# Kernel optimization log

Measured on AMD Instinct MI355X. Metric: run time of the kernel, lower is better.

## Reference

```python
import jax, jax.numpy as jnp
import numpy as np

N, E, G, D, L, EA = 100000, 1600000, 128, 128, 3, 7
BN_EPS = 1e-5


def _bn(x, g, b, m, v):
    # eval-mode BatchNorm1d with running stats
    return (x - m) * (g / jnp.sqrt(v + BN_EPS)) + b


def setup_inputs() -> dict:
    key = jax.random.key(0)
    ks = iter(jax.random.split(key, 64))
    nrm = lambda shape, s: jax.random.normal(next(ks), shape, jnp.float32) * s
    unif = lambda shape: jax.random.uniform(next(ks), shape, jnp.float32) * 0.5 + 0.5
    inp = {
        # forward tensor args
        'x': jnp.zeros((N,), jnp.int32),  # indices into Embedding(1, D) -> all zero
        'edge_index': jax.random.randint(next(ks), (2, E), 0, N, jnp.int32),
        'edge_attr': nrm((E, EA), 1.0),
        'batch': jnp.sort(jax.random.randint(next(ks), (N,), 0, G, jnp.int32)),
        # embeddings
        'node_emb': nrm((1, D), 1.0),
        'vn_emb': nrm((1, D), 0.1),
        # per-layer GINConv params (stacked on leading layer dim)
        'edge_W': nrm((L, EA, D), EA ** -0.5), 'edge_b': jnp.zeros((L, D), jnp.float32),
        'eps': jnp.zeros((L,), jnp.float32),
        'mlp_W1': nrm((L, D, 2 * D), D ** -0.5), 'mlp_b1': jnp.zeros((L, 2 * D), jnp.float32),
        'mbn_g': jnp.ones((L, 2 * D), jnp.float32), 'mbn_b': jnp.zeros((L, 2 * D), jnp.float32),
        'mbn_m': nrm((L, 2 * D), 0.1), 'mbn_v': unif((L, 2 * D)),
        'mlp_W2': nrm((L, 2 * D, D), (2 * D) ** -0.5), 'mlp_b2': jnp.zeros((L, D), jnp.float32),
        # outer per-layer BatchNorm
        'bn_g': jnp.ones((L, D), jnp.float32), 'bn_b': jnp.zeros((L, D), jnp.float32),
        'bn_m': nrm((L, D), 0.1), 'bn_v': unif((L, D)),
        # virtual-node MLPs (L-1 of them)
        'vn_W1': nrm((L - 1, D, 2 * D), D ** -0.5), 'vn_b1': jnp.zeros((L - 1, 2 * D), jnp.float32),
        'vbn1_g': jnp.ones((L - 1, 2 * D), jnp.float32), 'vbn1_b': jnp.zeros((L - 1, 2 * D), jnp.float32),
        'vbn1_m': nrm((L - 1, 2 * D), 0.1), 'vbn1_v': unif((L - 1, 2 * D)),
        'vn_W2': nrm((L - 1, 2 * D, D), (2 * D) ** -0.5), 'vn_b2': jnp.zeros((L - 1, D), jnp.float32),
        'vbn2_g': jnp.ones((L - 1, D), jnp.float32), 'vbn2_b': jnp.zeros((L - 1, D), jnp.float32),
        'vbn2_m': nrm((L - 1, D), 0.1), 'vbn2_v': unif((L - 1, D)),
    }
    return inp


def reference(x, edge_index, edge_attr, batch, node_emb, vn_emb,
              edge_W, edge_b, eps, mlp_W1, mlp_b1, mbn_g, mbn_b, mbn_m, mbn_v,
              mlp_W2, mlp_b2, bn_g, bn_b, bn_m, bn_v,
              vn_W1, vn_b1, vbn1_g, vbn1_b, vbn1_m, vbn1_v,
              vn_W2, vn_b2, vbn2_g, vbn2_b, vbn2_m, vbn2_v):
    src, dst = edge_index[0], edge_index[1]
    h = node_emb[x]                                # [N, D] node encoder gather
    vn = jnp.broadcast_to(vn_emb[0], (G, D))       # virtual node per graph
    for l in range(L):
        h_in = h + vn[batch]                       # broadcast virtual node to nodes
        # GINConv
        e = edge_attr @ edge_W[l] + edge_b[l]      # [E, D]
        msg = jax.nn.relu(h_in[src] + e)           # gather + edge fuse
        agg = jax.ops.segment_sum(msg, dst, num_segments=N)
        z = (1.0 + eps[l]) * h_in + agg
        z = jax.nn.relu(_bn(z @ mlp_W1[l] + mlp_b1[l], mbn_g[l], mbn_b[l], mbn_m[l], mbn_v[l]))
        h2 = z @ mlp_W2[l] + mlp_b2[l]
        # outer BatchNorm (+ relu except last layer; dropout is identity in eval)
        h2 = _bn(h2, bn_g[l], bn_b[l], bn_m[l], bn_v[l])
        h = h2 if l == L - 1 else jax.nn.relu(h2)
        if l < L - 1:
            vt = jax.ops.segment_sum(h_in, batch, num_segments=G) + vn  # global_add_pool
            t = jax.nn.relu(_bn(vt @ vn_W1[l] + vn_b1[l], vbn1_g[l], vbn1_b[l], vbn1_m[l], vbn1_v[l]))
            vn = jax.nn.relu(_bn(t @ vn_W2[l] + vn_b2[l], vbn2_g[l], vbn2_b[l], vbn2_m[l], vbn2_v[l]))
    return h  # JK == 'last'
```

## Files before the change

kernel.cpp:

```cpp
#include <hip/hip_runtime.h>
#include <hip/hip_bf16.h>

#define NN 100000
#define NP 100032
#define EE 1600000
#define GG 128
#define DD 128
#define LL 3
#define EAA 7
#define BN_EPS 1e-5f

typedef __attribute__((ext_vector_type(8))) short bf16x8;
typedef __attribute__((ext_vector_type(4))) float f32x4;
typedef __attribute__((ext_vector_type(4))) unsigned short u16x4;
typedef _Float16 f16x2 __attribute__((ext_vector_type(2)));

__device__ __forceinline__ unsigned short f2bf(float x) {
    unsigned int u = __float_as_uint(x);
    u = (u + 0x7FFF + ((u >> 16) & 1)) >> 16;
    return (unsigned short)u;
}
__device__ __forceinline__ float bf2f(unsigned short h) {
    return __uint_as_float(((unsigned int)h) << 16);
}
__device__ __forceinline__ float bflo(unsigned int u) {
    return __uint_as_float(u << 16);
}
__device__ __forceinline__ float bfhi(unsigned int u) {
    return __uint_as_float(u & 0xFFFF0000u);
}
__device__ __forceinline__ unsigned int pkf16(float a, float b) {
    f16x2 v = {(_Float16)a, (_Float16)b};
    return __builtin_bit_cast(unsigned int, v);
}
__device__ __forceinline__ unsigned short f16bits(float a) {
    _Float16 h = (_Float16)a;
    return __builtin_bit_cast(unsigned short, h);
}

#if __has_builtin(__builtin_amdgcn_fdot2)
#define DOT2(q, w, c) __builtin_amdgcn_fdot2((q), (w), (c), false)
#else
__device__ __forceinline__ float dot2_sw(f16x2 a, f16x2 b, float c) {
    return fmaf((float)a.x, (float)b.x, fmaf((float)a.y, (float)b.y, c));
}
#define DOT2(q, w, c) dot2_sw((q), (w), (c))
#endif

__global__ __launch_bounds__(256) void init_kernel(
    const int* __restrict__ x, const float* __restrict__ node_emb,
    const float* __restrict__ vn_emb, float* __restrict__ h,
    float* __restrict__ vn)
{
    long i = (long)blockIdx.x * 256 + threadIdx.x;
    if (i < (long)NN * DD) {
        int node = (int)(i >> 7), d = (int)(i & 127);
        h[i] = node_emb[(long)x[node] * DD + d];
    }
    if (i < GG * DD) vn[i] = vn_emb[i & 127];
}

#define R1 8
__global__ __launch_bounds__(256) void hin_kernel(
    float* __restrict__ hbuf,
    unsigned short* __restrict__ h16,
    const float* __restrict__ vn,
    const int* __restrict__ batch,
    const float* __restrict__ eps,
    float* __restrict__ agg,
    float* __restrict__ vt,
    int layer, int accum_vt, int write_agg)
{
    const int d  = threadIdx.x & 127;
    const int rg = threadIdx.x >> 7;
    const float epl = 1.0f + eps[layer];
    const long row0 = (long)blockIdx.x * (R1 * 2);

    float vacc = 0.0f;
    int   vb   = -1;
    #pragma unroll
    for (int r = 0; r < R1; ++r) {
        long row = row0 + rg + 2 * r;
        if (row >= NN) break;
        int b = batch[row];
        long idx = row * DD + d;
        float hv = hbuf[idx] + vn[(long)b * DD + d];
        hbuf[idx] = hv;
        h16[idx]  = f2bf(hv);
        if (write_agg) agg[idx] = epl * hv;
        if (accum_vt) {
            if (b != vb) {
                if (vb >= 0) atomicAdd(&vt[(long)vb * DD + d], vacc);
                vb = b; vacc = 0.0f;
            }
            vacc += hv;
        }
    }
    if (accum_vt && vb >= 0) atomicAdd(&vt[(long)vb * DD + d], vacc);
}

__global__ __launch_bounds__(256) void vt_kernel(
    const float* __restrict__ hbuf, const int* __restrict__ batch,
    float* __restrict__ vt)
{
    const int d  = threadIdx.x & 127;
    const int rg = threadIdx.x >> 7;
    const long row0 = (long)blockIdx.x * 16;
    float vacc = 0.0f;
    int   vb   = -1;
    #pragma unroll
    for (int r = 0; r < 8; ++r) {
        long row = row0 + rg + 2 * r;
        if (row >= NN) break;
        int b = batch[row];
        float hv = hbuf[row * DD + d];
        if (b != vb) {
            if (vb >= 0) atomicAdd(&vt[(long)vb * DD + d], vacc);
            vb = b; vacc = 0.0f;
        }
        vacc += hv;
    }
    if (vb >= 0) atomicAdd(&vt[(long)vb * DD + d], vacc);
}

__global__ __launch_bounds__(256) void cnt_kernel(
    const int* __restrict__ batch, int* __restrict__ cnt)
{
    const int tid = blockIdx.x * 256 + threadIdx.x;
    const int CH  = (NN + 16383) / 16384;
    long s = (long)tid * CH;
    long e = s + CH; if (e > NN) e = NN;
    int vb = -1, c = 0;
    for (long i = s; i < e; ++i) {
        int b = batch[i];
        if (b != vb) { if (vb >= 0) atomicAdd(&cnt[vb], c); vb = b; c = 0; }
        ++c;
    }
    if (vb >= 0) atomicAdd(&cnt[vb], c);
}

__global__ __launch_bounds__(256) void count_kernel(
    const int* __restrict__ ei, int* __restrict__ deg)
{
    long e = (long)blockIdx.x * 256 + threadIdx.x;
    if (e < EE) atomicAdd(&deg[ei[EE + e]], 1);
}

__global__ __launch_bounds__(1024) void scan_a(
    const int* __restrict__ deg, int* __restrict__ rp, int* __restrict__ partials)
{
    __shared__ int s[1024];
    int t = threadIdx.x;
    long i = (long)blockIdx.x * 1024 + t;
    int v = (i < NN) ? deg[i] : 0;
    s[t] = v;
    __syncthreads();
    for (int off = 1; off < 1024; off <<= 1) {
        int u = (t >= off) ? s[t - off] : 0;
        __syncthreads();
        s[t] += u;
        __syncthreads();
    }
    if (i < NN) rp[i] = s[t] - v;
    if (t == 1023) partials[blockIdx.x] = s[1023];
}

__global__ void scan_b(int* __restrict__ partials, int nb)
{
    if (threadIdx.x == 0) {
        int run = 0;
        for (int i = 0; i < nb; ++i) { int v = partials[i]; partials[i] = run; run += v; }
    }
}

__global__ __launch_bounds__(1024) void scan_c(
    int* __restrict__ rp, int* __restrict__ fill, const int* __restrict__ partials)
{
    long i = (long)blockIdx.x * 1024 + threadIdx.x;
    if (i < NN) {
        int v = rp[i] + partials[blockIdx.x];
        rp[i] = v;
        fill[i] = v;
    }
    if (i == 0) rp[NN] = EE;
}

__global__ __launch_bounds__(256) void scatter_kernel(
    const int* __restrict__ ei, const float* __restrict__ eattr,
    int* __restrict__ fill, unsigned int* __restrict__ attr16,
    int* __restrict__ eid_perm)
{
    long e = (long)blockIdx.x * 256 + threadIdx.x;
    if (e >= EE) return;
    int dst = ei[EE + e];
    int pos = atomicAdd(&fill[dst], 1);
    if (attr16) {
        unsigned int src = (unsigned int)ei[e];
        uint4 w;
        w.x = pkf16(eattr[e * EAA + 0], eattr[e * EAA + 1]);
        w.y = pkf16(eattr[e * EAA + 2], eattr[e * EAA + 3]);
        w.z = pkf16(eattr[e * EAA + 4], eattr[e * EAA + 5]);
        unsigned int a6 = (unsigned int)f16bits(eattr[e * EAA + 6]) & 0xFFFEu;
        w.w = a6 | ((src >> 16) & 1u) | (src << 16);
        *(uint4*)(attr16 + (long)pos * 4) = w;
    } else {
        eid_perm[pos] = (int)e;
    }
}

#define WPAIR_PREAMBLE(eWl)                                                   \
    f16x2 wx[4], wy[4];                                                       \
    {                                                                         \
        _Pragma("unroll")                                                     \
        for (int j = 0; j < 3; ++j) {                                         \
            float2 p0 = *(const float2*)&(eWl)[(2 * j) * DD + d0];            \
            float2 p1 = *(const float2*)&(eWl)[(2 * j + 1) * DD + d0];        \
            wx[j] = (f16x2){(_Float16)p0.x, (_Float16)p1.x};                  \
            wy[j] = (f16x2){(_Float16)p0.y, (_Float16)p1.y};                  \
        }                                                                     \
        float2 p6 = *(const float2*)&(eWl)[6 * DD + d0];                      \
        wx[3] = (f16x2){(_Float16)p6.x, (_Float16)0.0f};                      \
        wy[3] = (f16x2){(_Float16)p6.y, (_Float16)0.0f};                      \
    }

#define EDOT(AU, EX, EY)                                                      \
    float EX = bias.x, EY = bias.y;                                           \
    {                                                                         \
        f16x2 q0 = __builtin_bit_cast(f16x2, AU.x);                           \
        f16x2 q1 = __builtin_bit_cast(f16x2, AU.y);                           \
        f16x2 q2 = __builtin_bit_cast(f16x2, AU.z);                           \
        f16x2 q3 = __builtin_bit_cast(f16x2, AU.w & 0x0000FFFEu);             \
        EX = DOT2(q0, wx[0], EX); EY = DOT2(q0, wy[0], EY);                   \
        EX = DOT2(q1, wx[1], EX); EY = DOT2(q1, wy[1], EY);                   \
        EX = DOT2(q2, wx[2], EX); EY = DOT2(q2, wy[2], EY);                   \
        EX = DOT2(q3, wx[3], EX); EY = DOT2(q3, wy[3], EY);                   \
    }

#define UNPACK_SRC(AW) (int)(((AW) >> 16) | (((AW) & 1u) << 16))

__global__ __launch_bounds__(256) void gin0_kernel(
    const float* __restrict__ node_emb,
    const float* __restrict__ vn_emb,
    const int* __restrict__ rp,
    const unsigned int* __restrict__ attr16,
    const float* __restrict__ eW, const float* __restrict__ eb,
    const float* __restrict__ eps,
    unsigned short* __restrict__ aggh, unsigned short* __restrict__ aggl)
{
    const int lane = threadIdx.x & 63;
    const int wid  = __builtin_amdgcn_readfirstlane(threadIdx.x >> 6);
    const int n    = blockIdx.x * 4 + wid;
    const int d0   = lane * 2;

    WPAIR_PREAMBLE(eW)
    const float2 bias = *(const float2*)&eb[d0];
    const float  epl  = 1.0f + eps[0];

    const float cx = node_emb[d0]     + vn_emb[d0];
    const float cy = node_emb[d0 + 1] + vn_emb[d0 + 1];
    float accx = epl * cx, accy = epl * cy;

    int p        = __builtin_amdgcn_readfirstlane(rp[n]);
    const int p1 = __builtin_amdgcn_readfirstlane(rp[n + 1]);

    #define EDGE0(AU)                                                         \
    {                                                                         \
        EDOT(AU, ex, ey)                                                      \
        float mx = cx + ex, my = cy + ey;                                     \
        accx += fmaxf(mx, 0.0f); accy += fmaxf(my, 0.0f);                     \
    }

    for (; p + 4 <= p1; p += 4) {
        const uint4* a4p = (const uint4*)(attr16 + (long)p * 4);
        uint4 A0 = a4p[0];
        uint4 A1 = a4p[1];
        uint4 A2 = a4p[2];
        uint4 A3 = a4p[3];
        EDGE0(A0)
        EDGE0(A1)
        EDGE0(A2)
        EDGE0(A3)
    }
    for (; p < p1; ++p) {
        uint4 A = *(const uint4*)(attr16 + (long)p * 4);
        EDGE0(A)
    }
    #undef EDGE0

    unsigned short hx = f2bf(accx), hy = f2bf(accy);
    *(unsigned int*)&aggh[(long)n * DD + d0] = (unsigned int)hx | ((unsigned int)hy << 16);
    *(unsigned int*)&aggl[(long)n * DD + d0] =
        (unsigned int)f2bf(accx - bf2f(hx)) | ((unsigned int)f2bf(accy - bf2f(hy)) << 16);
}

__global__ __launch_bounds__(256) void gin_agg_kernel(
    const float* __restrict__ h_in,
    const unsigned short* __restrict__ h16,
    const int* __restrict__ rp,
    const unsigned int* __restrict__ attr16,
    const float* __restrict__ eW, const float* __restrict__ eb,
    const float* __restrict__ eps,
    unsigned short* __restrict__ aggh, unsigned short* __restrict__ aggl,
    int layer)
{
    const int lane = threadIdx.x & 63;
    const int wid  = __builtin_amdgcn_readfirstlane(threadIdx.x >> 6);
    const int n    = blockIdx.x * 4 + wid;
    const int d0   = lane * 2;

    const float* eWl = eW + (long)layer * EAA * DD;
    WPAIR_PREAMBLE(eWl)
    const float2 bias = *(const float2*)&eb[layer * DD + d0];
    const float  epl  = 1.0f + eps[layer];

    float2 hn = *(const float2*)&h_in[(long)n * DD + d0];
    float accx = epl * hn.x, accy = epl * hn.y;

    int p        = __builtin_amdgcn_readfirstlane(rp[n]);
    const int p1 = __builtin_amdgcn_readfirstlane(rp[n + 1]);

    #define EDGE(AU, GU)                                                      \
    {                                                                         \
        EDOT(AU, ex, ey)                                                      \
        float mx = bflo(GU) + ex, my = bfhi(GU) + ey;                         \
        accx += fmaxf(mx, 0.0f); accy += fmaxf(my, 0.0f);                     \
    }

    for (; p + 4 <= p1; p += 4) {
        const uint4* a4p = (const uint4*)(attr16 + (long)p * 4);
        uint4 A0 = a4p[0];
        uint4 A1 = a4p[1];
        uint4 A2 = a4p[2];
        uint4 A3 = a4p[3];
        int s0 = __builtin_amdgcn_readfirstlane(UNPACK_SRC(A0.w));
        int s1 = __builtin_amdgcn_readfirstlane(UNPACK_SRC(A1.w));
        int s2 = __builtin_amdgcn_readfirstlane(UNPACK_SRC(A2.w));
        int s3 = __builtin_amdgcn_readfirstlane(UNPACK_SRC(A3.w));
        unsigned int g0 = *(const unsigned int*)(h16 + (long)s0 * DD + d0);
        unsigned int g1 = *(const unsigned int*)(h16 + (long)s1 * DD + d0);
        unsigned int g2 = *(const unsigned int*)(h16 + (long)s2 * DD + d0);
        unsigned int g3 = *(const unsigned int*)(h16 + (long)s3 * DD + d0);
        EDGE(A0, g0)
        EDGE(A1, g1)
        EDGE(A2, g2)
        EDGE(A3, g3)
    }
    for (; p < p1; ++p) {
        uint4 A = *(const uint4*)(attr16 + (long)p * 4);
        int s = __builtin_amdgcn_readfirstlane(UNPACK_SRC(A.w));
        unsigned int g = *(const unsigned int*)(h16 + (long)s * DD + d0);
        EDGE(A, g)
    }
    #undef EDGE

    unsigned short hx = f2bf(accx), hy = f2bf(accy);
    *(unsigned int*)&aggh[(long)n * DD + d0] = (unsigned int)hx | ((unsigned int)hy << 16);
    *(unsigned int*)&aggl[(long)n * DD + d0] =
        (unsigned int)f2bf(accx - bf2f(hx)) | ((unsigned int)f2bf(accy - bf2f(hy)) << 16);
}

__global__ __launch_bounds__(256) void gin_agg_eid_kernel(
    const float* __restrict__ h_in,
    const int* __restrict__ rp,
    const int* __restrict__ eid_perm,
    const int* __restrict__ ei,
    const float* __restrict__ eattr,
    const float* __restrict__ eW, const float* __restrict__ eb,
    const float* __restrict__ eps,
    float* __restrict__ agg, int layer)
{
    const int d    = threadIdx.x & 127;
    const int half = threadIdx.x >> 7;
    const long n   = (long)blockIdx.x * 2 + half;

    float w[EAA];
    #pragma unroll
    for (int a = 0; a < EAA; ++a) w[a] = eW[layer * EAA * DD + a * DD + d];
    const float bias = eb[layer * DD + d];
    const float epl  = 1.0f + eps[layer];

    float acc = epl * h_in[n * DD + d];
    const int p0 = rp[n], p1 = rp[n + 1];
    for (int p = p0; p < p1; ++p) {
        int e = eid_perm[p];
        int src = ei[e];
        float ea = bias;
        #pragma unroll
        for (int a = 0; a < EAA; ++a)
            ea = fmaf(eattr[(long)e * EAA + a], w[a], ea);
        float m = h_in[(long)src * DD + d] + ea;
        acc += m > 0.0f ? m : 0.0f;
    }
    agg[n * DD + d] = acc;
}

__global__ __launch_bounds__(256) void wprep_kernel(
    const float* __restrict__ W1, const float* __restrict__ W2,
    unsigned short* __restrict__ w1h, unsigned short* __restrict__ w1l,
    unsigned short* __restrict__ w2h, unsigned short* __restrict__ w2l)
{
    int tid = blockIdx.x * 256 + threadIdx.x;
    if (tid >= LL * 2 * 32768) return;
    int l = tid / 65536;
    int rem = tid - l * 65536;
    int mat = rem >> 15;
    int fi = rem & 32767;
    int b = fi & 7, lane = (fi >> 3) & 63;
    int kgrp = ((lane >> 4) << 3) + b;
    if (mat == 0) {
        int mt = (fi >> 9) & 15, kk = fi >> 13;
        int m = (mt << 4) + (lane & 15);
        int k = (kk << 5) + kgrp;
        float v = W1[(long)l * DD * 2 * DD + (long)k * 2 * DD + m];
        unsigned short hi = f2bf(v);
        w1h[(long)l * 32768 + fi] = hi;
        w1l[(long)l * 32768 + fi] = f2bf(v - bf2f(hi));
    } else {
        int mt = (fi >> 9) & 7, kk = fi >> 12;
        int m = (mt << 4) + (lane & 15);
        int k = (kk << 5) + kgrp;
        float v = W2[(long)l * 2 * DD * DD + (long)k * DD + m];
        unsigned short hi = f2bf(v);
        w2h[(long)l * 32768 + fi] = hi;
        w2l[(long)l * 32768 + fi] = f2bf(v - bf2f(hi));
    }
}

__global__ __launch_bounds__(256) void bnprep_kernel(
    const float* __restrict__ b1, const float* __restrict__ g1,
    const float* __restrict__ be1, const float* __restrict__ m1,
    const float* __restrict__ v1,
    const float* __restrict__ b2, const float* __restrict__ g2,
    const float* __restrict__ be2, const float* __restrict__ m2,
    const float* __restrict__ v2,
    float* __restrict__ sc1, float* __restrict__ sh1,
    float* __restrict__ sc2, float* __restrict__ sh2)
{
    int tid = blockIdx.x * 256 + threadIdx.x;
    if (tid < LL * 2 * DD) {
        float sc = g1[tid] / sqrtf(v1[tid] + BN_EPS);
        sc1[tid] = sc;
        sh1[tid] = (b1[tid] - m1[tid]) * sc + be1[tid];
    }
    int t2 = tid - LL * 2 * DD;
    if (t2 >= 0 && t2 < LL * DD) {
        float sc = g2[t2] / sqrtf(v2[t2] + BN_EPS);
        sc2[t2] = sc;
        sh2[t2] = (b2[t2] - m2[t2]) * sc + be2[t2];
    }
}

__global__ __launch_bounds__(256, 2) void mlp_mfma_kernel(
    const float* __restrict__ z_in,
    const unsigned short* __restrict__ z16h, const unsigned short* __restrict__ z16l,
    int zfmt,
    const unsigned short* __restrict__ w1h, const unsigned short* __restrict__ w1l,
    const unsigned short* __restrict__ w2h, const unsigned short* __restrict__ w2l,
    const float* __restrict__ sc1, const float* __restrict__ sh1,
    const float* __restrict__ sc2, const float* __restrict__ sh2,
    float* __restrict__ h_out, int layer, int do_relu,
    const int* __restrict__ batch, const float* __restrict__ vnbuf,
    unsigned short* __restrict__ h16, int fuse)
{
    __shared__ char lds[65536];
    const int tid  = threadIdx.x;
    const int lane = tid & 63;
    const int wv   = tid >> 6;
    const long row0 = (long)blockIdx.x * 64;
    const int kb = (lane >> 4) << 3;

    if (zfmt) {
        const uint4* zh = (const uint4*)(z16h + row0 * DD);
        const uint4* zl = (const uint4*)(z16l + row0 * DD);
        #pragma unroll
        for (int i = 0; i < 4; ++i) {
            int idx = tid + i * 256;
            uint4 hv = zh[idx];
            uint4 lv = zl[idx];
            int r = idx >> 4;
            int c = (idx & 15) << 3;
            int off = ((r << 8) + (c << 1)) ^ ((r & 7) << 4);
            *(uint4*)(lds + off)         = hv;
            *(uint4*)(lds + 16384 + off) = lv;
        }
    } else {
        const float4* zi = (const float4*)(z_in + row0 * DD);
        #pragma unroll
        for (int i = 0; i < 8; ++i) {
            int idx = tid + i * 256;
            float4 v = zi[idx];
            int r = idx >> 5;
            int c = (idx & 31) << 2;
            u16x4 hv, lv;
            hv.x = f2bf(v.x); lv.x = f2bf(v.x - bf2f(hv.x));
            hv.y = f2bf(v.y); lv.y = f2bf(v.y - bf2f(hv.y));
            hv.z = f2bf(v.z); lv.z = f2bf(v.z - bf2f(hv.z));
            hv.w = f2bf(v.w); lv.w = f2bf(v.w - bf2f(hv.w));
            int off = ((r << 8) + (c << 1)) ^ ((r & 7) << 4);
            *(u16x4*)(lds + off)         = hv;
            *(u16x4*)(lds + 16384 + off) = lv;
        }
    }
    __syncthreads();

    bf16x8 B1h[4][4], B1l[4][4];
    #pragma unroll
    for (int nt = 0; nt < 4; ++nt) {
        int r = (nt << 4) + (lane & 15);
        #pragma unroll
        for (int kk = 0; kk < 4; ++kk) {
            int off = ((r << 8) + (((kk << 5) + kb) << 1)) ^ ((r & 7) << 4);
            B1h[nt][kk] = *(const bf16x8*)(lds + off);
            B1l[nt][kk] = *(const bf16x8*)(lds + 16384 + off);
        }
    }
    __syncthreads();

    const unsigned short* w1hl = w1h + (long)layer * 32768;
    const unsigned short* w1ll = w1l + (long)layer * 32768;
    #pragma unroll
    for (int mtl = 0; mtl < 4; ++mtl) {
        const int mt = (wv << 2) + mtl;
        bf16x8 Ah[4], Al[4];
        #pragma unroll
        for (int kk = 0; kk < 4; ++kk) {
            const long boff = ((long)((kk << 4) + mt) * 64 + lane) << 3;
            Ah[kk] = *(const bf16x8*)(w1hl + boff);
            Al[kk] = *(const bf16x8*)(w1ll + boff);
        }
        f32x4 acc[4];
        #pragma unroll
        for (int nt = 0; nt < 4; ++nt) acc[nt] = (f32x4){0.f, 0.f, 0.f, 0.f};
        #pragma unroll
        for (int kk = 0; kk < 4; ++kk) {
            #pragma unroll
            for (int nt = 0; nt < 4; ++nt) {
                acc[nt] = __builtin_amdgcn_mfma_f32_16x16x32_bf16(Ah[kk], B1h[nt][kk], acc[nt], 0, 0, 0);
                acc[nt] = __builtin_amdgcn_mfma_f32_16x16x32_bf16(Ah[kk], B1l[nt][kk], acc[nt], 0, 0, 0);
                acc[nt] = __builtin_amdgcn_mfma_f32_16x16x32_bf16(Al[kk], B1h[nt][kk], acc[nt], 0, 0, 0);
            }
        }
        const int m0 = (mt << 4) + ((lane >> 4) << 2);
        const float4 s4 = *(const float4*)&sc1[layer * 2 * DD + m0];
        const float4 t4 = *(const float4*)&sh1[layer * 2 * DD + m0];
        #pragma unroll
        for (int nt = 0; nt < 4; ++nt) {
            int row = (nt << 4) + (lane & 15);
            float u0 = fmaxf(fmaf(acc[nt][0], s4.x, t4.x), 0.0f);
            float u1 = fmaxf(fmaf(acc[nt][1], s4.y, t4.y), 0.0f);
            float u2 = fmaxf(fmaf(acc[nt][2], s4.z, t4.z), 0.0f);
            float u3 = fmaxf(fmaf(acc[nt][3], s4.w, t4.w), 0.0f);
            u16x4 hv, lv;
            hv.x = f2bf(u0); lv.x = f2bf(u0 - bf2f(hv.x));
            hv.y = f2bf(u1); lv.y = f2bf(u1 - bf2f(hv.y));
            hv.z = f2bf(u2); lv.z = f2bf(u2 - bf2f(hv.z));
            hv.w = f2bf(u3); lv.w = f2bf(u3 - bf2f(hv.w));
            int off = ((row << 9) + (m0 << 1)) ^ ((row & 7) << 4);
            *(u16x4*)(lds + off)         = hv;
            *(u16x4*)(lds + 32768 + off) = lv;
        }
    }
    __syncthreads();

    const unsigned short* w2hl = w2h + (long)layer * 32768;
    const unsigned short* w2ll = w2l + (long)layer * 32768;
    f32x4 acc2[2][4];
    #pragma unroll
    for (int mtl = 0; mtl < 2; ++mtl)
        #pragma unroll
        for (int nt = 0; nt < 4; ++nt) acc2[mtl][nt] = (f32x4){0.f, 0.f, 0.f, 0.f};

    #pragma unroll
    for (int kk = 0; kk < 8; ++kk) {
        bf16x8 Bh[4], Bl[4];
        #pragma unroll
        for (int nt = 0; nt < 4; ++nt) {
            int r = (nt << 4) + (lane & 15);
            int off = ((r << 9) + (((kk << 5) + kb) << 1)) ^ ((r & 7) << 4);
            Bh[nt] = *(const bf16x8*)(lds + off);
            Bl[nt] = *(const bf16x8*)(lds + 32768 + off);
        }
        #pragma unroll
        for (int mtl = 0; mtl < 2; ++mtl) {
            const int mt = (wv << 1) + mtl;
            const long boff = ((long)((kk << 3) + mt) * 64 + lane) << 3;
            bf16x8 Ah = *(const bf16x8*)(w2hl + boff);
            bf16x8 Al = *(const bf16x8*)(w2ll + boff);
            #pragma unroll
            for (int nt = 0; nt < 4; ++nt) {
                acc2[mtl][nt] = __builtin_amdgcn_mfma_f32_16x16x32_bf16(Ah, Bh[nt], acc2[mtl][nt], 0, 0, 0);
                acc2[mtl][nt] = __builtin_amdgcn_mfma_f32_16x16x32_bf16(Ah, Bl[nt], acc2[mtl][nt], 0, 0, 0);
                acc2[mtl][nt] = __builtin_amdgcn_mfma_f32_16x16x32_bf16(Al, Bh[nt], acc2[mtl][nt], 0, 0, 0);
            }
        }
    }
    #pragma unroll
    for (int mtl = 0; mtl < 2; ++mtl) {
        const int m0 = ((((wv << 1) + mtl)) << 4) + ((lane >> 4) << 2);
        const float4 s4 = *(const float4*)&sc2[layer * DD + m0];
        const float4 t4 = *(const float4*)&sh2[layer * DD + m0];
        #pragma unroll
        for (int nt = 0; nt < 4; ++nt) {
            long row = row0 + (nt << 4) + (lane & 15);
            if (row < NN) {
                float o0 = fmaf(acc2[mtl][nt][0], s4.x, t4.x);
                float o1 = fmaf(acc2[mtl][nt][1], s4.y, t4.y);
                float o2 = fmaf(acc2[mtl][nt][2], s4.z, t4.z);
                float o3 = fmaf(acc2[mtl][nt][3], s4.w, t4.w);
                if (do_relu) {
                    o0 = fmaxf(o0, 0.0f); o1 = fmaxf(o1, 0.0f);
                    o2 = fmaxf(o2, 0.0f); o3 = fmaxf(o3, 0.0f);
                }
                if (fuse) {
                    int b = batch[row];
                    float4 vnv = *(const float4*)&vnbuf[(long)b * DD + m0];
                    o0 += vnv.x; o1 += vnv.y; o2 += vnv.z; o3 += vnv.w;
                    u16x4 hv;
                    hv.x = f2bf(o0); hv.y = f2bf(o1);
                    hv.z = f2bf(o2); hv.w = f2bf(o3);
                    *(u16x4*)&h16[row * DD + m0] = hv;
                }
                *(float4*)&h_out[row * DD + m0] = make_float4(o0, o1, o2, o3);
            }
        }
    }
}

__global__ __launch_bounds__(256) void vn_kernel(
    const float* __restrict__ vt, float* __restrict__ vn,
    const float* __restrict__ W1, const float* __restrict__ b1,
    const float* __restrict__ g1, const float* __restrict__ be1,
    const float* __restrict__ m1, const float* __restrict__ v1,
    const float* __restrict__ W2, const float* __restrict__ b2,
    const float* __restrict__ g2, const float* __restrict__ be2,
    const float* __restrict__ m2, const float* __restrict__ v2,
    int layer)
{
    __shared__ float row[DD];
    __shared__ float u[2 * DD];
    const int g = blockIdx.x;
    const int t = threadIdx.x;

    if (t < DD) row[t] = vt[(long)g * DD + t] + vn[(long)g * DD + t];
    __syncthreads();

    {
        const float* W = W1 + (long)layer * DD * 2 * DD;
        float acc = 0.0f;
        for (int k = 0; k < DD; ++k) acc = fmaf(row[k], W[k * 2 * DD + t], acc);
        const long o = (long)layer * 2 * DD + t;
        float sc = g1[o] / sqrtf(v1[o] + BN_EPS);
        float sh = be1[o] - m1[o] * sc;
        float val = (acc + b1[o]) * sc + sh;
        u[t] = val > 0.0f ? val : 0.0f;
    }
    __syncthreads();

    if (t < DD) {
        const float* W = W2 + (long)layer * 2 * DD * DD;
        float acc = 0.0f;
        for (int k = 0; k < 2 * DD; ++k) acc = fmaf(u[k], W[k * DD + t], acc);
        const long o = (long)layer * DD + t;
        float sc = g2[o] / sqrtf(v2[o] + BN_EPS);
        float sh = be2[o] - m2[o] * sc;
        float val = (acc + b2[o]) * sc + sh;
        vn[(long)g * DD + t] = val > 0.0f ? val : 0.0f;
    }
}

__global__ __launch_bounds__(256) void vn0_kernel(
    const int* __restrict__ cnt,
    const float* __restrict__ node_emb, const float* __restrict__ vn_emb,
    float* __restrict__ vn,
    const float* __restrict__ W1, const float* __restrict__ b1,
    const float* __restrict__ g1, const float* __restrict__ be1,
    const float* __restrict__ m1, const float* __restrict__ v1,
    const float* __restrict__ W2, const float* __restrict__ b2,
    const float* __restrict__ g2, const float* __restrict__ be2,
    const float* __restrict__ m2, const float* __restrict__ v2)
{
    __shared__ float row[DD];
    __shared__ float u[2 * DD];
    const int g = blockIdx.x;
    const int t = threadIdx.x;

    if (t < DD) {
        float c = node_emb[t] + vn_emb[t];
        row[t] = (float)cnt[g] * c + vn_emb[t];
    }
    __syncthreads();

    {
        float acc = 0.0f;
        for (int k = 0; k < DD; ++k) acc = fmaf(row[k], W1[k * 2 * DD + t], acc);
        float sc = g1[t] / sqrtf(v1[t] + BN_EPS);
        float sh = be1[t] - m1[t] * sc;
        float val = (acc + b1[t]) * sc + sh;
        u[t] = val > 0.0f ? val : 0.0f;
    }
    __syncthreads();

    if (t < DD) {
        float acc = 0.0f;
        for (int k = 0; k < 2 * DD; ++k) acc = fmaf(u[k], W2[k * DD + t], acc);
        float sc = g2[t] / sqrtf(v2[t] + BN_EPS);
        float sh = be2[t] - m2[t] * sc;
        float val = (acc + b2[t]) * sc + sh;
        vn[(long)g * DD + t] = val > 0.0f ? val : 0.0f;
    }
}

extern "C" void kernel_launch(void* const* d_in, const int* in_sizes, int n_in,
                              void* d_out, int out_size, void* d_ws, size_t ws_size,
                              hipStream_t stream)
{
    const int*   x       = (const int*)  d_in[0];
    const int*   ei      = (const int*)  d_in[1];
    const float* eattr   = (const float*)d_in[2];
    const int*   batch   = (const int*)  d_in[3];
    const float* node_emb= (const float*)d_in[4];
    const float* vn_emb  = (const float*)d_in[5];
    const float* edge_W  = (const float*)d_in[6];
    const float* edge_b  = (const float*)d_in[7];
    const float* eps     = (const float*)d_in[8];
    const float* mlp_W1  = (const float*)d_in[9];
    const float* mlp_b1  = (const float*)d_in[10];
    const float* mbn_g   = (const float*)d_in[11];
    const float* mbn_b   = (const float*)d_in[12];
    const float* mbn_m   = (const float*)d_in[13];
    const float* mbn_v   = (const float*)d_in[14];
    const float* mlp_W2  = (const float*)d_in[15];
    const float* mlp_b2  = (const float*)d_in[16];
    const float* bn_g    = (const float*)d_in[17];
    const float* bn_b    = (const float*)d_in[18];
    const float* bn_m    = (const float*)d_in[19];
    const float* bn_v    = (const float*)d_in[20];
    const float* vn_W1   = (const float*)d_in[21];
    const float* vn_b1   = (const float*)d_in[22];
    const float* vbn1_g  = (const float*)d_in[23];
    const float* vbn1_b  = (const float*)d_in[24];
    const float* vbn1_m  = (const float*)d_in[25];
    const float* vbn1_v  = (const float*)d_in[26];
    const float* vn_W2   = (const float*)d_in[27];
    const float* vn_b2   = (const float*)d_in[28];
    const float* vbn2_g  = (const float*)d_in[29];
    const float* vbn2_b  = (const float*)d_in[30];
    const float* vbn2_m  = (const float*)d_in[31];
    const float* vbn2_v  = (const float*)d_in[32];

    float* h = (float*)d_out;
    char*  ws = (char*)d_ws;

    size_t off = 0;
    auto alloc = [&](size_t bytes) -> void* {
        void* p = ws + off;
        off += (bytes + 255) & ~(size_t)255;
        return p;
    };
    const size_t GDB = (size_t)GG * DD * sizeof(float);

    float* agg      = (float*)alloc((size_t)NP * DD * sizeof(float));
    unsigned short* aggh = (unsigned short*)agg;
    unsigned short* aggl = aggh + (size_t)NP * DD;
    unsigned short* h16 = (unsigned short*)alloc((size_t)NN * DD * sizeof(unsigned short));
    float* vn       = (float*)alloc(GDB);
    float* vt       = (float*)alloc(GDB);
    int*   rp       = (int*)  alloc((NN + 1) * sizeof(int));
    int*   fill     = (int*)  alloc(NN * sizeof(int));
    int*   partials = (int*)  alloc(128 * sizeof(int));
    int*   cnt      = (int*)  alloc(GG * sizeof(int));
    unsigned short* w1h = (unsigned short*)alloc(LL * 32768 * sizeof(unsigned short));
    unsigned short* w1l = (unsigned short*)alloc(LL * 32768 * sizeof(unsigned short));
    unsigned short* w2h = (unsigned short*)alloc(LL * 32768 * sizeof(unsigned short));
    unsigned short* w2l = (unsigned short*)alloc(LL * 32768 * sizeof(unsigned short));
    float* bn1sc = (float*)alloc(LL * 2 * DD * sizeof(float));
    float* bn1sh = (float*)alloc(LL * 2 * DD * sizeof(float));
    float* bn2sc = (float*)alloc(LL * DD * sizeof(float));
    float* bn2sh = (float*)alloc(LL * DD * sizeof(float));
    const size_t base_end = off;

    unsigned int* attr16 = nullptr;
    int* eid_perm = nullptr;
    if (ws_size >= base_end + (size_t)EE * 4 * sizeof(unsigned int))
        attr16 = (unsigned int*)alloc((size_t)EE * 4 * sizeof(unsigned int));
    else if (ws_size >= base_end + (size_t)EE * sizeof(int))
        eid_perm = (int*)alloc((size_t)EE * sizeof(int));
    const bool csr = (attr16 != nullptr) || (eid_perm != nullptr);

    wprep_kernel<<<(LL * 2 * 32768 + 255) / 256, 256, 0, stream>>>(
        mlp_W1, mlp_W2, w1h, w1l, w2h, w2l);
    bnprep_kernel<<<(LL * 2 * DD + LL * DD + 255) / 256, 256, 0, stream>>>(
        mlp_b1, mbn_g, mbn_b, mbn_m, mbn_v,
        mlp_b2, bn_g, bn_b, bn_m, bn_v,
        bn1sc, bn1sh, bn2sc, bn2sh);

    if (csr) {
        const int egrid = (EE + 255) / 256;
        const int ngrid = (NN + 1023) / 1024;
        hipMemsetAsync(fill, 0, NN * sizeof(int), stream);
        count_kernel<<<egrid, 256, 0, stream>>>(ei, fill);
        scan_a<<<ngrid, 1024, 0, stream>>>(fill, rp, partials);
        scan_b<<<1, 64, 0, stream>>>(partials, ngrid);
        scan_c<<<ngrid, 1024, 0, stream>>>(rp, fill, partials);
        scatter_kernel<<<egrid, 256, 0, stream>>>(ei, eattr, fill, attr16, eid_perm);
    }

    if (attr16) {
        hipMemsetAsync(cnt, 0, GG * sizeof(int), stream);
        cnt_kernel<<<64, 256, 0, stream>>>(batch, cnt);

        vn0_kernel<<<GG, 256, 0, stream>>>(
            cnt, node_emb, vn_emb, vn,
            vn_W1, vn_b1, vbn1_g, vbn1_b, vbn1_m, vbn1_v,
            vn_W2, vn_b2, vbn2_g, vbn2_b, vbn2_m, vbn2_v);
        gin0_kernel<<<NN / 4, 256, 0, stream>>>(
            node_emb, vn_emb, rp, attr16, edge_W, edge_b, eps, aggh, aggl);
        mlp_mfma_kernel<<<NP / 64, 256, 0, stream>>>(
            agg, aggh, aggl, 1, w1h, w1l, w2h, w2l, bn1sc, bn1sh, bn2sc, bn2sh,
            h, 0, 1, batch, vn, h16, 1);

        hipMemsetAsync(vt, 0, GDB, stream);
        vt_kernel<<<NN / 16, 256, 0, stream>>>(h, batch, vt);
        vn_kernel<<<GG, 256, 0, stream>>>(
            vt, vn, vn_W1, vn_b1, vbn1_g, vbn1_b, vbn1_m, vbn1_v,
            vn_W2, vn_b2, vbn2_g, vbn2_b, vbn2_m, vbn2_v, 1);
        gin_agg_kernel<<<NN / 4, 256, 0, stream>>>(
            h, h16, rp, attr16, edge_W, edge_b, eps, aggh, aggl, 1);
        mlp_mfma_kernel<<<NP / 64, 256, 0, stream>>>(
            agg, aggh, aggl, 1, w1h, w1l, w2h, w2l, bn1sc, bn1sh, bn2sc, bn2sh,
            h, 1, 1, batch, vn, h16, 1);

        gin_agg_kernel<<<NN / 4, 256, 0, stream>>>(
            h, h16, rp, attr16, edge_W, edge_b, eps, aggh, aggl, 2);
        mlp_mfma_kernel<<<NP / 64, 256, 0, stream>>>(
            agg, aggh, aggl, 1, w1h, w1l, w2h, w2l, bn1sc, bn1sh, bn2sc, bn2sh,
            h, 2, 0, batch, vn, h16, 0);
    } else {
        {
            long total = (long)NN * DD;
            init_kernel<<<(int)((total + 255) / 256), 256, 0, stream>>>(
                x, node_emb, vn_emb, h, vn);
        }
        for (int l = 0; l < LL; ++l) {
            int accum = (l < LL - 1) ? 1 : 0;
            if (accum)
                hipMemsetAsync(vt, 0, GDB, stream);

            hin_kernel<<<NN / (R1 * 2), 256, 0, stream>>>(
                h, h16, vn, batch, eps, agg, vt, l, accum, 1);

            if (eid_perm) {
                gin_agg_eid_kernel<<<NN / 2, 256, 0, stream>>>(
                    h, rp, eid_perm, ei, eattr, edge_W, edge_b, eps, agg, l);
            }

            mlp_mfma_kernel<<<NP / 64, 256, 0, stream>>>(
                agg, nullptr, nullptr, 0, w1h, w1l, w2h, w2l,
                bn1sc, bn1sh, bn2sc, bn2sh,
                h, l, accum, batch, vn, h16, 0);

            if (accum)
                vn_kernel<<<GG, 256, 0, stream>>>(
                    vt, vn, vn_W1, vn_b1, vbn1_g, vbn1_b, vbn1_m, vbn1_v,
                    vn_W2, vn_b2, vbn2_g, vbn2_b, vbn2_m, vbn2_v, l);
        }
    }
}
```

Before: 662.1 us.

## Bin CSR edge scatter by destination range and store source ids separately

Replaces the single-pass edge scatter with a binned scatter. Each block walks one chunk of edges and only handles edges whose destination falls in one of 8 node ranges, so the atomics and scattered writes for a block stay within a small region of memory that is more likely to stay in cache. Source indices now go to their own int array instead of being bit-packed into the edge-attribute word, and the aggregation kernel reads them with a vector load. In exchange, the destination array is read eight times, and each aggregation layer does an extra index load per edge.

Measured after the change: 657.0 us. No clear change (-0.8%).

```diff
diff --git a/kernel.cpp b/kernel.cpp
--- a/kernel.cpp
+++ b/kernel.cpp
@@ -9,6 +9,8 @@
 #define LL 3
 #define EAA 7
 #define BN_EPS 1e-5f
+#define NBIN 8
+#define BINW 12500
 
 typedef __attribute__((ext_vector_type(8))) short bf16x8;
 typedef __attribute__((ext_vector_type(4))) float f32x4;
@@ -32,10 +34,6 @@
 __device__ __forceinline__ unsigned int pkf16(float a, float b) {
     f16x2 v = {(_Float16)a, (_Float16)b};
     return __builtin_bit_cast(unsigned int, v);
-}
-__device__ __forceinline__ unsigned short f16bits(float a) {
-    _Float16 h = (_Float16)a;
-    return __builtin_bit_cast(unsigned short, h);
 }
 
 #if __has_builtin(__builtin_amdgcn_fdot2)
@@ -185,27 +183,40 @@
     if (i == 0) rp[NN] = EE;
 }
 
-__global__ __launch_bounds__(256) void scatter_kernel(
+#define P2C 8192
+__global__ __launch_bounds__(256) void binscat_kernel(
     const int* __restrict__ ei, const float* __restrict__ eattr,
-    int* __restrict__ fill, unsigned int* __restrict__ attr16,
+    int* __restrict__ fill,
+    unsigned int* __restrict__ attr16, int* __restrict__ src_arr)
+{
+    const int b  = blockIdx.x & 7;
+    const long e0 = (long)(blockIdx.x >> 3) * P2C;
+    const int lo = b * BINW, hi = lo + BINW;
+    long e1 = e0 + P2C; if (e1 > EE) e1 = EE;
+    for (long e = e0 + threadIdx.x; e < e1; e += 256) {
+        int dst = ei[EE + e];
+        if (dst >= lo && dst < hi) {
+            int q = atomicAdd(&fill[dst], 1);
+            uint4 w;
+            w.x = pkf16(eattr[e * EAA + 0], eattr[e * EAA + 1]);
+            w.y = pkf16(eattr[e * EAA + 2], eattr[e * EAA + 3]);
+            w.z = pkf16(eattr[e * EAA + 4], eattr[e * EAA + 5]);
+            w.w = pkf16(eattr[e * EAA + 6], 0.0f);
+            *(uint4*)(attr16 + (long)q * 4) = w;
+            src_arr[q] = ei[e];
+        }
+    }
+}
+
+__global__ __launch_bounds__(256) void scatter_eid_kernel(
+    const int* __restrict__ ei, int* __restrict__ fill,
     int* __restrict__ eid_perm)
 {
     long e = (long)blockIdx.x * 256 + threadIdx.x;
     if (e >= EE) return;
     int dst = ei[EE + e];
     int pos = atomicAdd(&fill[dst], 1);
-    if (attr16) {
-        unsigned int src = (unsigned int)ei[e];
-        uint4 w;
-        w.x = pkf16(eattr[e * EAA + 0], eattr[e * EAA + 1]);
-        w.y = pkf16(eattr[e * EAA + 2], eattr[e * EAA + 3]);
-        w.z = pkf16(eattr[e * EAA + 4], eattr[e * EAA + 5]);
-        unsigned int a6 = (unsigned int)f16bits(eattr[e * EAA + 6]) & 0xFFFEu;
-        w.w = a6 | ((src >> 16) & 1u) | (src << 16);
-        *(uint4*)(attr16 + (long)pos * 4) = w;
-    } else {
-        eid_perm[pos] = (int)e;
-    }
+    eid_perm[pos] = (int)e;
 }
 
 #define WPAIR_PREAMBLE(eWl)                                                   \
@@ -229,14 +240,12 @@
         f16x2 q0 = __builtin_bit_cast(f16x2, AU.x);                           \
         f16x2 q1 = __builtin_bit_cast(f16x2, AU.y);                           \
         f16x2 q2 = __builtin_bit_cast(f16x2, AU.z);                           \
-        f16x2 q3 = __builtin_bit_cast(f16x2, AU.w & 0x0000FFFEu);             \
+        f16x2 q3 = __builtin_bit_cast(f16x2, AU.w);                           \
         EX = DOT2(q0, wx[0], EX); EY = DOT2(q0, wy[0], EY);                   \
         EX = DOT2(q1, wx[1], EX); EY = DOT2(q1, wy[1], EY);                   \
         EX = DOT2(q2, wx[2], EX); EY = DOT2(q2, wy[2], EY);                   \
         EX = DOT2(q3, wx[3], EX); EY = DOT2(q3, wy[3], EY);                   \
     }
-
-#define UNPACK_SRC(AW) (int)(((AW) >> 16) | (((AW) & 1u) << 16))
 
 __global__ __launch_bounds__(256) void gin0_kernel(
     const float* __restrict__ node_emb,
@@ -298,6 +307,7 @@
     const unsigned short* __restrict__ h16,
     const int* __restrict__ rp,
     const unsigned int* __restrict__ attr16,
+    const int* __restrict__ src_arr,
     const float* __restrict__ eW, const float* __restrict__ eb,
     const float* __restrict__ eps,
     unsigned short* __restrict__ aggh, unsigned short* __restrict__ aggl,
@@ -327,15 +337,16 @@
     }
 
     for (; p + 4 <= p1; p += 4) {
+        int4 sv = *(const int4*)(src_arr + p);
+        int s0 = __builtin_amdgcn_readfirstlane(sv.x);
+        int s1 = __builtin_amdgcn_readfirstlane(sv.y);
+        int s2 = __builtin_amdgcn_readfirstlane(sv.z);
+        int s3 = __builtin_amdgcn_readfirstlane(sv.w);
         const uint4* a4p = (const uint4*)(attr16 + (long)p * 4);
         uint4 A0 = a4p[0];
         uint4 A1 = a4p[1];
         uint4 A2 = a4p[2];
         uint4 A3 = a4p[3];
-        int s0 = __builtin_amdgcn_readfirstlane(UNPACK_SRC(A0.w));
-        int s1 = __builtin_amdgcn_readfirstlane(UNPACK_SRC(A1.w));
-        int s2 = __builtin_amdgcn_readfirstlane(UNPACK_SRC(A2.w));
-        int s3 = __builtin_amdgcn_readfirstlane(UNPACK_SRC(A3.w));
         unsigned int g0 = *(const unsigned int*)(h16 + (long)s0 * DD + d0);
         unsigned int g1 = *(const unsigned int*)(h16 + (long)s1 * DD + d0);
         unsigned int g2 = *(const unsigned int*)(h16 + (long)s2 * DD + d0);
@@ -346,8 +357,8 @@
         EDGE(A3, g3)
     }
     for (; p < p1; ++p) {
+        int s = __builtin_amdgcn_readfirstlane(src_arr[p]);
         uint4 A = *(const uint4*)(attr16 + (long)p * 4);
-        int s = __builtin_amdgcn_readfirstlane(UNPACK_SRC(A.w));
         unsigned int g = *(const unsigned int*)(h16 + (long)s * DD + d0);
         EDGE(A, g)
     }
@@ -769,6 +780,7 @@
     int*   fill     = (int*)  alloc(NN * sizeof(int));
     int*   partials = (int*)  alloc(128 * sizeof(int));
     int*   cnt      = (int*)  alloc(GG * sizeof(int));
+    int*   src_arr  = (int*)  alloc((size_t)EE * sizeof(int));
     unsigned short* w1h = (unsigned short*)alloc(LL * 32768 * sizeof(unsigned short));
     unsigned short* w1l = (unsigned short*)alloc(LL * 32768 * sizeof(unsigned short));
     unsigned short* w2h = (unsigned short*)alloc(LL * 32768 * sizeof(unsigned short));
@@ -780,12 +792,9 @@
     const size_t base_end = off;
 
     unsigned int* attr16 = nullptr;
-    int* eid_perm = nullptr;
     if (ws_size >= base_end + (size_t)EE * 4 * sizeof(unsigned int))
         attr16 = (unsigned int*)alloc((size_t)EE * 4 * sizeof(unsigned int));
-    else if (ws_size >= base_end + (size_t)EE * sizeof(int))
-        eid_perm = (int*)alloc((size_t)EE * sizeof(int));
-    const bool csr = (attr16 != nullptr) || (eid_perm != nullptr);
+    int* eid_perm = src_arr;
 
     wprep_kernel<<<(LL * 2 * 32768 + 255) / 256, 256, 0, stream>>>(
         mlp_W1, mlp_W2, w1h, w1l, w2h, w2l);
@@ -794,7 +803,7 @@
         mlp_b2, bn_g, bn_b, bn_m, bn_v,
         bn1sc, bn1sh, bn2sc, bn2sh);
 
-    if (csr) {
+    {
         const int egrid = (EE + 255) / 256;
         const int ngrid = (NN + 1023) / 1024;
         hipMemsetAsync(fill, 0, NN * sizeof(int), stream);
@@ -802,7 +811,13 @@
         scan_a<<<ngrid, 1024, 0, stream>>>(fill, rp, partials);
         scan_b<<<1, 64, 0, stream>>>(partials, ngrid);
         scan_c<<<ngrid, 1024, 0, stream>>>(rp, fill, partials);
-        scatter_kernel<<<egrid, 256, 0, stream>>>(ei, eattr, fill, attr16, eid_perm);
+        if (attr16) {
+            const int chunks = (EE + P2C - 1) / P2C;
+            binscat_kernel<<<NBIN * chunks, 256, 0, stream>>>(
+                ei, eattr, fill, attr16, src_arr);
+        } else {
+            scatter_eid_kernel<<<egrid, 256, 0, stream>>>(ei, fill, eid_perm);
+        }
     }
 
     if (attr16) {
@@ -825,13 +840,13 @@
             vt, vn, vn_W1, vn_b1, vbn1_g, vbn1_b, vbn1_m, vbn1_v,
             vn_W2, vn_b2, vbn2_g, vbn2_b, vbn2_m, vbn2_v, 1);
         gin_agg_kernel<<<NN / 4, 256, 0, stream>>>(
-            h, h16, rp, attr16, edge_W, edge_b, eps, aggh, aggl, 1);
+            h, h16, rp, attr16, src_arr, edge_W, edge_b, eps, aggh, aggl, 1);
         mlp_mfma_kernel<<<NP / 64, 256, 0, stream>>>(
             agg, aggh, aggl, 1, w1h, w1l, w2h, w2l, bn1sc, bn1sh, bn2sc, bn2sh,
             h, 1, 1, batch, vn, h16, 1);
 
         gin_agg_kernel<<<NN / 4, 256, 0, stream>>>(
-            h, h16, rp, attr16, edge_W, edge_b, eps, aggh, aggl, 2);
+            h, h16, rp, attr16, src_arr, edge_W, edge_b, eps, aggh, aggl, 2);
         mlp_mfma_kernel<<<NP / 64, 256, 0, stream>>>(
             agg, aggh, aggl, 1, w1h, w1l, w2h, w2l, bn1sc, bn1sh, bn2sc, bn2sh,
             h, 2, 0, batch, vn, h16, 0);
@@ -849,10 +864,8 @@
             hin_kernel<<<NN / (R1 * 2), 256, 0, stream>>>(
                 h, h16, vn, batch, eps, agg, vt, l, accum, 1);
 
-            if (eid_perm) {
-                gin_agg_eid_kernel<<<NN / 2, 256, 0, stream>>>(
-                    h, rp, eid_perm, ei, eattr, edge_W, edge_b, eps, agg, l);
-            }
+            gin_agg_eid_kernel<<<NN / 2, 256, 0, stream>>>(
+                h, rp, eid_perm, ei, eattr, edge_W, edge_b, eps, agg, l);
 
             mlp_mfma_kernel<<<NP / 64, 256, 0, stream>>>(
                 agg, nullptr, nullptr, 0, w1h, w1l, w2h, w2l,
```
